# Optimization experiments

Measured on AMD Instinct MI355X. Metric: run time of the kernel, lower is better.

## Reference

```python
import jax, jax.numpy as jnp
import numpy as np

NUM_HEADS = 16
NUM_KV_HEADS = 4
HEAD_DIM = 256
ROPE_THETA = 10000.0


def _rope(x, position_ids):
    # x: [B, H, S, D], position_ids: [B, S]
    d = x.shape[-1]
    inv_freq = 1.0 / (ROPE_THETA ** (jnp.arange(0, d, 2, dtype=jnp.float32) / d))  # [D/2]
    freqs = position_ids.astype(jnp.float32)[:, :, None] * inv_freq[None, None, :]  # [B, S, D/2]
    emb = jnp.concatenate([freqs, freqs], axis=-1)  # [B, S, D]
    cos = jnp.cos(emb)[:, None, :, :]
    sin = jnp.sin(emb)[:, None, :, :]
    x1, x2 = jnp.split(x, 2, axis=-1)
    rot = jnp.concatenate([-x2, x1], axis=-1)
    return x * cos + rot * sin


def setup_inputs() -> dict:
    key = jax.random.key(0)
    k1, k2, k3, k4, k5 = jax.random.split(key, 5)
    B, S, H = 2, 2048, 2048
    hidden_states = jax.random.normal(k1, (B, S, H), dtype=jnp.float32)
    position_ids = jnp.broadcast_to(jnp.arange(S, dtype=jnp.int32)[None, :], (B, S))
    scale = 1.0 / np.sqrt(H)
    wq = jax.random.normal(k2, (H, NUM_HEADS * HEAD_DIM), dtype=jnp.float32) * scale
    wk = jax.random.normal(k3, (H, NUM_KV_HEADS * HEAD_DIM), dtype=jnp.float32) * scale
    wv = jax.random.normal(k4, (H, NUM_KV_HEADS * HEAD_DIM), dtype=jnp.float32) * scale
    wo = jax.random.normal(k5, (NUM_HEADS * HEAD_DIM, H), dtype=jnp.float32) * (1.0 / np.sqrt(NUM_HEADS * HEAD_DIM))
    return {"hidden_states": hidden_states, "position_ids": position_ids,
            "wq": wq, "wk": wk, "wv": wv, "wo": wo}


def reference(hidden_states, position_ids, wq, wk, wv, wo):
    B, S, H = hidden_states.shape
    groups = NUM_HEADS // NUM_KV_HEADS
    # QKV projections -> [B, heads, S, D]
    q = (hidden_states @ wq).reshape(B, S, NUM_HEADS, HEAD_DIM).transpose(0, 2, 1, 3)
    k = (hidden_states @ wk).reshape(B, S, NUM_KV_HEADS, HEAD_DIM).transpose(0, 2, 1, 3)
    v = (hidden_states @ wv).reshape(B, S, NUM_KV_HEADS, HEAD_DIM).transpose(0, 2, 1, 3)
    q = _rope(q, position_ids)
    k = _rope(k, position_ids)
    # GQA without materializing repeated K/V: group query heads per kv head
    qg = q.reshape(B, NUM_KV_HEADS, groups, S, HEAD_DIM)
    scale = 1.0 / jnp.sqrt(jnp.asarray(HEAD_DIM, dtype=q.dtype))
    scores = jnp.einsum('bkgqd,bkvd->bkgqv', qg, k) * scale  # [B, KV, G, S, S]
    causal = jnp.tril(jnp.ones((S, S), dtype=bool))
    scores = jnp.where(causal[None, None, None, :, :], scores, jnp.finfo(scores.dtype).min)
    probs = jax.nn.softmax(scores, axis=-1)
    out = jnp.einsum('bkgqv,bkvd->bkgqd', probs, v)  # [B, KV, G, S, D]
    out = out.reshape(B, NUM_HEADS, S, HEAD_DIM).transpose(0, 2, 1, 3).reshape(B, S, NUM_HEADS * HEAD_DIM)
    return out @ wo
```

## Files before the change

kernel.cpp:

```cpp
#include <hip/hip_runtime.h>

typedef unsigned short u16;
typedef __bf16 bf16_t;
typedef bf16_t bf16x8 __attribute__((ext_vector_type(8)));
typedef float f32x4 __attribute__((ext_vector_type(4)));
typedef float f32x16 __attribute__((ext_vector_type(16)));

#define LOG2E 1.4426950408889634f
#define QKVS 6144

__device__ __forceinline__ u16 f2bf(float f) {
  union { float f; unsigned u; } c; c.f = f;
  unsigned r = c.u + 0x7fffu + ((c.u >> 16) & 1u);
  return (u16)(r >> 16);
}
__device__ __forceinline__ float bf2f(u16 u) {
  union { unsigned u; float f; } c; c.u = ((unsigned)u) << 16;
  return c.f;
}

__device__ __forceinline__ void gload16(const void* g, void* l) {
  __builtin_amdgcn_global_load_lds(
      (const __attribute__((address_space(1))) unsigned int*)g,
      (__attribute__((address_space(3))) unsigned int*)l, 16, 0, 0);
}

__device__ __forceinline__ unsigned cvtpk(float lo, float hi) {
  unsigned r;
  asm("v_cvt_pk_bf16_f32 %0, %1, %2" : "=v"(r) : "v"(lo), "v"(hi));
  return r;
}
__device__ __forceinline__ void swap32(unsigned& a, unsigned& b) {
  asm("v_permlane32_swap_b32 %0, %1" : "+v"(a), "+v"(b));
}

#define MFMA16(a, b, c) __builtin_amdgcn_mfma_f32_16x16x32_bf16((a), (b), (c), 0, 0, 0)
#define MFMA32(a, b, c) __builtin_amdgcn_mfma_f32_32x32x16_bf16((a), (b), (c), 0, 0, 0)


__global__ __launch_bounds__(256) void k_convert_f32_bf16(const float* __restrict__ in,
                                                          u16* __restrict__ out, int n4) {
  int i = blockIdx.x * 256 + threadIdx.x;
  if (i >= n4) return;
  float4 v = ((const float4*)in)[i];
  ushort4 o;
  o.x = f2bf(v.x); o.y = f2bf(v.y); o.z = f2bf(v.z); o.w = f2bf(v.w);
  ((ushort4*)out)[i] = o;
}

__global__ __launch_bounds__(256) void k_transpose_all(const float* __restrict__ wq,
                                                       const float* __restrict__ wk,
                                                       const float* __restrict__ wv,
                                                       const float* __restrict__ wo,
                                                       u16* __restrict__ Wqkvt,
                                                       u16* __restrict__ Wot) {
  __shared__ float tile[32][33];
  int fb = blockIdx.x;
  const float* in;
  u16* out;
  int R, C, bxi, byi;
  if (fb < 8192) {
    in = wq; out = Wqkvt; R = 2048; C = 4096;
    bxi = fb & 127; byi = fb >> 7;
  } else if (fb < 10240) {
    in = wk; out = Wqkvt + 4096 * 2048; R = 2048; C = 1024;
    int l = fb - 8192; bxi = l & 31; byi = l >> 5;
  } else if (fb < 12288) {
    in = wv; out = Wqkvt + 5120 * 2048; R = 2048; C = 1024;
    int l = fb - 10240; bxi = l & 31; byi = l >> 5;
  } else {
    in = wo; out = Wot; R = 4096; C = 2048;
    int l = fb - 12288; bxi = l & 63; byi = l >> 6;
  }
  int tx = threadIdx.x & 31, ty = threadIdx.x >> 5;
  int bx = bxi * 32, by = byi * 32;
#pragma unroll
  for (int i = 0; i < 4; i++)
    tile[ty + i * 8][tx] = in[(size_t)(by + ty + i * 8) * C + bx + tx];
  __syncthreads();
#pragma unroll
  for (int i = 0; i < 4; i++)
    out[(size_t)(bx + ty + i * 8) * R + by + tx] = f2bf(tile[tx][ty + i * 8]);
}

__global__ __launch_bounds__(256) void k_transpose_bf16(const u16* __restrict__ in,
                                                        u16* __restrict__ out, int R, int C) {
  __shared__ u16 tile[32][33];
  int tx = threadIdx.x, ty = threadIdx.y;
  int bx = blockIdx.x * 32, by = blockIdx.y * 32;
#pragma unroll
  for (int i = 0; i < 4; i++)
    tile[ty + i * 8][tx] = in[(size_t)(by + ty + i * 8) * C + bx + tx];
  __syncthreads();
#pragma unroll
  for (int i = 0; i < 4; i++)
    out[(size_t)(bx + ty + i * 8) * R + by + tx] = tile[tx][ty + i * 8];
}

__global__ __launch_bounds__(256) void k_ropetab(const int* __restrict__ pos,
                                                 float2* __restrict__ tab) {
  int idx = blockIdx.x * 256 + threadIdx.x;
  int i = idx & 127, row = idx >> 7;
  float p = (float)pos[row];
  float f = p * exp2f((float)i * (-13.287712379549449f / 128.f));
  float sn, cs;
  sincosf(f, &sn, &cs);
  tab[idx] = make_float2(cs, sn);
}


template <int OUT_BF16>
__global__ __launch_bounds__(256) void k_gemm_bt(const u16* __restrict__ A,
                                                 const u16* __restrict__ Bt,
                                                 void* __restrict__ C, int M, int N, int K) {
  __shared__ u16 As[128 * 64];
  __shared__ u16 Bs[128 * 64];
  const int tid = threadIdx.x;
  const int lane = tid & 63;
  const int w = tid >> 6;
  const int l15 = lane & 15, l4 = lane >> 4;
  const int wr = w >> 1, wc = w & 1;
  const int bx = blockIdx.x, by = blockIdx.y;

  f32x4 acc[4][4];
#pragma unroll
  for (int a = 0; a < 4; a++)
#pragma unroll
    for (int b2 = 0; b2 < 4; b2++) acc[a][b2] = (f32x4){0.f, 0.f, 0.f, 0.f};

  const u16* Abase = A + (size_t)by * 128 * K;
  const u16* Bbase = Bt + (size_t)bx * 128 * K;

  for (int kk = 0; kk < K; kk += 64) {
    __syncthreads();
#pragma unroll
    for (int j = 0; j < 4; j++) {
      int ci = w * 256 + j * 64 + lane;
      int row = ci >> 3, c = ci & 7;
      gload16(Abase + (size_t)row * K + kk + c * 8, (char*)As + ci * 16);
      gload16(Bbase + (size_t)row * K + kk + c * 8, (char*)Bs + ci * 16);
    }
    __syncthreads();
#pragma unroll
    for (int kc = 0; kc < 2; kc++) {
      int kb = kc * 64 + l4 * 16;
      bf16x8 av[4], bv[4];
#pragma unroll
      for (int mt = 0; mt < 4; mt++)
        av[mt] = *(const bf16x8*)((const char*)As + (wr * 64 + mt * 16 + l15) * 128 + kb);
#pragma unroll
      for (int nt = 0; nt < 4; nt++)
        bv[nt] = *(const bf16x8*)((const char*)Bs + (wc * 64 + nt * 16 + l15) * 128 + kb);
#pragma unroll
      for (int mt = 0; mt < 4; mt++)
#pragma unroll
        for (int nt = 0; nt < 4; nt++) acc[mt][nt] = MFMA16(av[mt], bv[nt], acc[mt][nt]);
    }
  }
#pragma unroll
  for (int mt = 0; mt < 4; mt++) {
#pragma unroll
    for (int nt = 0; nt < 4; nt++) {
      int col = bx * 128 + wc * 64 + nt * 16 + l15;
#pragma unroll
      for (int r = 0; r < 4; r++) {
        int row = by * 128 + wr * 64 + mt * 16 + l4 * 4 + r;
        if (OUT_BF16)
          ((u16*)C)[(size_t)row * N + col] = f2bf(acc[mt][nt][r]);
        else
          ((float*)C)[(size_t)row * N + col] = acc[mt][nt][r];
      }
    }
  }
}


__global__ __launch_bounds__(512, 1) void k_gemm256(const u16* __restrict__ A,
                                                    const u16* __restrict__ Bt,
                                                    u16* __restrict__ C, int N, int K,
                                                    const float2* __restrict__ tab) {
  extern __shared__ char smem[];
  const int tid = threadIdx.x;
  const int lane = tid & 63, w = tid >> 6;
  const int l15 = lane & 15, l4 = lane >> 4;
  const int wr = w >> 2, wc = w & 3;
  const int bx = blockIdx.x, by = blockIdx.y;
  const int NT = K >> 6;

  const u16* Ab = A + (size_t)(by * 256) * K;
  const u16* Bb = Bt + (size_t)(bx * 256) * K;

  int srcoff[2], dstoff[2];
#pragma unroll
  for (int rr = 0; rr < 2; rr++) {
    int ci = rr * 512 + tid;
    int lc = ci ^ (((ci >> 5) & 1) << 1);
    int kc = lc >> 9, row = (lc >> 2) & 127, g2 = lc & 3;
    srcoff[rr] = row * K + kc * 32 + g2 * 8;
    dstoff[rr] = ci * 16;
  }

  auto SH = [&](int Tg, int halfidx) {
    const u16* base = (halfidx < 2) ? (Ab + (size_t)(halfidx * 128) * K)
                                    : (Bb + (size_t)((halfidx - 2) * 128) * K);
    char* dst = smem + (Tg & 1) * 65536 + halfidx * 16384;
    int kk = Tg * 64;
#pragma unroll
    for (int rr = 0; rr < 2; rr++)
      gload16(base + srcoff[rr] + kk, dst + dstoff[rr]);
  };

  auto lda = [&](int c, int kc, int mrow4) -> bf16x8 {
    int L = kc * 8192 + (mrow4 * 16 + l15) * 64 + l4 * 16;
    int P = L ^ (((L >> 9) & 1) << 5);
    return *(const bf16x8*)(smem + c * 65536 + wr * 16384 + P);
  };
  auto ldb = [&](int c, int kc, int j) -> bf16x8 {
    int L = kc * 8192 + ((wc & 1) * 64 + j * 16 + l15) * 64 + l4 * 16;
    int P = L ^ (((L >> 9) & 1) << 5);
    return *(const bf16x8*)(smem + c * 65536 + 32768 + (wc >> 1) * 16384 + P);
  };

  f32x4 acc[8][4];
#pragma unroll
  for (int i = 0; i < 8; i++)
#pragma unroll
    for (int j = 0; j < 4; j++) acc[i][j] = (f32x4){0.f, 0.f, 0.f, 0.f};

  SH(0, 0); SH(0, 1); SH(0, 2); SH(0, 3);
  SH(1, 2); SH(1, 3);
  asm volatile("s_waitcnt vmcnt(4)" ::: "memory");
  __builtin_amdgcn_s_barrier();
  asm volatile("" ::: "memory");

  bf16x8 bv[2][4];
  for (int T = 0; T < NT; ++T) {
    const int c = T & 1;
#pragma unroll
    for (int q = 0; q < 4; q++) {
      const int kc = q & 1, mh = q >> 1;
      bf16x8 av[4];
      if (q < 2) {
#pragma unroll
        for (int j = 0; j < 4; j++) bv[kc][j] = ldb(c, kc, j);
      }
#pragma unroll
      for (int ii = 0; ii < 4; ii++) av[ii] = lda(c, kc, mh * 4 + ii);
      if (q == 0)      { if (T + 1 < NT) SH(T + 1, 0); }
      else if (q == 1) { if (T + 1 < NT) SH(T + 1, 1); }
      else if (q == 2) { if (T + 2 < NT) SH(T + 2, 2); }
      else             { if (T + 2 < NT) SH(T + 2, 3); }
      if (q == 3) {
        if (T < NT - 2)       asm volatile("s_waitcnt vmcnt(4)" ::: "memory");
        else if (T == NT - 2) asm volatile("s_waitcnt vmcnt(0)" ::: "memory");
      }
      asm volatile("" ::: "memory");
      __builtin_amdgcn_s_barrier();
      asm volatile("" ::: "memory");
      asm volatile("s_waitcnt lgkmcnt(0)" ::: "memory");
      __builtin_amdgcn_sched_barrier(0);
      __builtin_amdgcn_s_setprio(1);
#pragma unroll
      for (int ii = 0; ii < 4; ii++)
#pragma unroll
        for (int j = 0; j < 4; j++)
          acc[mh * 4 + ii][j] = MFMA16(av[ii], bv[kc][j], acc[mh * 4 + ii][j]);
      __builtin_amdgcn_s_setprio(0);
      asm volatile("" ::: "memory");
      __builtin_amdgcn_s_barrier();
      asm volatile("" ::: "memory");
    }
  }

  if (bx < 20) {
    float4* X4 = (float4*)smem;
    const float sgn = (wc < 2) ? -1.f : 1.f;
    const int ptid = tid ^ 128;
#pragma unroll
    for (int ih = 0; ih < 2; ih++) {
      __syncthreads();
#pragma unroll
      for (int i2 = 0; i2 < 4; i2++)
#pragma unroll
        for (int j2 = 0; j2 < 4; j2++) {
          f32x4 a = acc[ih * 4 + i2][j2];
          X4[(i2 * 4 + j2) * 512 + tid] = make_float4(a[0], a[1], a[2], a[3]);
        }
      __syncthreads();
#pragma unroll
      for (int i2 = 0; i2 < 4; i2++) {
#pragma unroll
        for (int j2 = 0; j2 < 4; j2++) {
          int col = bx * 256 + wc * 64 + j2 * 16 + l15;
          int ti = (wc & 1) * 64 + j2 * 16 + l15;
          float4 part = X4[(i2 * 4 + j2) * 512 + ptid];
          float pa[4] = {part.x, part.y, part.z, part.w};
#pragma unroll
          for (int r2 = 0; r2 < 4; r2++) {
            int row = by * 256 + wr * 128 + (ih * 4 + i2) * 16 + l4 * 4 + r2;
            float mine = acc[ih * 4 + i2][j2][r2];
            float2 t = tab[(size_t)row * 128 + ti];
            C[(size_t)row * N + col] = f2bf(mine * t.x + sgn * pa[r2] * t.y);
          }
        }
      }
    }
  } else {
#pragma unroll
    for (int i = 0; i < 8; i++) {
#pragma unroll
      for (int j = 0; j < 4; j++) {
        int col = bx * 256 + wc * 64 + j * 16 + l15;
#pragma unroll
        for (int r = 0; r < 4; r++) {
          int row = by * 256 + wr * 128 + i * 16 + l4 * 4 + r;
          C[(size_t)row * N + col] = f2bf(acc[i][j][r]);
        }
      }
    }
  }
}


__shared__ __align__(16) u16 aK0[8192];
__shared__ __align__(16) u16 aK1[8192];
__shared__ __align__(16) u16 aV0[8192];
__shared__ __align__(16) u16 aV1[8192];

__global__ __launch_bounds__(256, 2) void k_attn(const u16* __restrict__ QKV,
                                                 const u16* __restrict__ Vt,
                                                 u16* __restrict__ AO) {
  const int tid = threadIdx.x, lane = tid & 63, w = tid >> 6;
  const int r31 = lane & 31, hi = lane >> 5;

  const int flat = blockIdx.x;
  const int r = flat & 7;
  const int idx = flat >> 3;
  const int b = r >> 2, kv = r & 3;
  const int half = idx >> 5, j = idx & 31;
  const int qb = half ? 15 - (j >> 1) : (j >> 1);
  const int h = kv * 4 + (j & 1) + 2 * half;

  bf16x8 qreg[16];
  {
    const u16* qp = QKV + (size_t)(b * 2048 + qb * 128 + w * 32 + r31) * QKVS + h * 256 + hi * 8;
#pragma unroll
    for (int kc = 0; kc < 16; kc++) qreg[kc] = *(const bf16x8*)(qp + kc * 16);
  }

  f32x16 o[8];
#pragma unroll
  for (int df = 0; df < 8; df++)
#pragma unroll
    for (int jj = 0; jj < 16; jj++) o[df][jj] = 0.f;
  float mrow = -3e38f, lrow = 0.f;

  const int nt = 4 * qb + 4;
  const int tlim = 4 * qb + w;
  const int qloc = qb * 128 + w * 32 + r31;
  const u16* Kbase = QKV + (size_t)(b * 2048) * QKVS + 4096 + kv * 256;
  const u16* Vbase = Vt + (size_t)(kv * 256) * 4096 + b * 2048;

  int kfix[4], vfix[4];
#pragma unroll
  for (int jj = 0; jj < 4; jj++) {
    int ci = jj * 256 + tid;
    int krow = ci >> 5, kc = ci & 31;
    int kcg = (kc & 24) | ((kc ^ krow) & 7);
    kfix[jj] = krow * QKVS + kcg * 8;
    int vrow = ci >> 2, vc = ci & 3;
    int vg = (vc - (vrow >> 1)) & 3;
    vfix[jj] = vrow * 4096 + vg * 8;
  }
  int koff = 0, voff = 0;

  auto STAGE = [&](u16* Kd, u16* Vd) {
#pragma unroll
    for (int jj = 0; jj < 4; jj++)
      gload16(Kbase + kfix[jj] + koff, (char*)Kd + (jj * 256 + tid) * 16);
#pragma unroll
    for (int jj = 0; jj < 4; jj++)
      gload16(Vbase + vfix[jj] + voff, (char*)Vd + (jj * 256 + tid) * 16);
    koff += 32 * QKVS;
    voff += 32;
  };

  auto COMPUTE = [&](int t, const u16* Kc, const u16* Vc) {
    f32x16 s;
#pragma unroll
    for (int jj = 0; jj < 16; jj++) s[jj] = 0.f;
#pragma unroll
    for (int kc = 0; kc < 16; kc++) {
      int ch = kc * 2 + hi;
      int cs = (ch & 24) | ((ch ^ r31) & 7);
      bf16x8 kf = *(const bf16x8*)((const char*)Kc + r31 * 512 + cs * 16);
      s = MFMA32(kf, qreg[kc], s);
    }

    const float C = 0.0625f * LOG2E;
    float z[16];
#pragma unroll
    for (int jj = 0; jj < 16; jj++) z[jj] = s[jj] * C;
    if (t == tlim) {
#pragma unroll
      for (int jj = 0; jj < 16; jj++) {
        int kvg = t * 32 + (jj & 3) + 8 * (jj >> 2) + 4 * hi;
        if (kvg > qloc) z[jj] = -1e30f;
      }
    }

    float m0 = z[0];
#pragma unroll
    for (int jj = 1; jj < 16; jj++) m0 = fmaxf(m0, z[jj]);
    m0 = fmaxf(m0, __shfl_xor(m0, 32));
    if (__any(m0 > mrow + 11.54f)) {
      float mn = fmaxf(mrow, m0);
      float alpha = exp2f(mrow - mn);
      mrow = mn;
      lrow *= alpha;
#pragma unroll
      for (int jj = 0; jj < 16; jj++) {
        float a = __shfl(alpha, (jj & 3) + 8 * (jj >> 2) + 4 * hi);
#pragma unroll
        for (int df = 0; df < 8; df++) o[df][jj] *= a;
      }
    }
    float sum = 0.f;
#pragma unroll
    for (int jj = 0; jj < 16; jj++) {
      z[jj] = exp2f(z[jj] - mrow);
      sum += z[jj];
    }
    sum += __shfl_xor(sum, 32);
    lrow += sum;

    unsigned a0 = cvtpk(z[0], z[1]), a2 = cvtpk(z[4], z[5]);
    swap32(a0, a2);
    unsigned a1 = cvtpk(z[2], z[3]), a3 = cvtpk(z[6], z[7]);
    swap32(a1, a3);
    unsigned b0 = cvtpk(z[8], z[9]), b2 = cvtpk(z[12], z[13]);
    swap32(b0, b2);
    unsigned b1 = cvtpk(z[10], z[11]), b3 = cvtpk(z[14], z[15]);
    swap32(b1, b3);
    union UU { unsigned u[4]; bf16x8 v; };
    UU ua; ua.u[0] = a0; ua.u[1] = a1; ua.u[2] = a2; ua.u[3] = a3;
    UU ub; ub.u[0] = b0; ub.u[1] = b1; ub.u[2] = b2; ub.u[3] = b3;
    bf16x8 pa0 = ua.v, pa1 = ub.v;

#pragma unroll
    for (int df = 0; df < 8; df++) {
      int vr = df * 32 + r31;
      int c0 = (hi + (vr >> 1)) & 3;
      int c1 = (2 + hi + (vr >> 1)) & 3;
      bf16x8 v0 = *(const bf16x8*)((const char*)Vc + vr * 64 + c0 * 16);
      bf16x8 v1 = *(const bf16x8*)((const char*)Vc + vr * 64 + c1 * 16);
      o[df] = MFMA32(pa0, v0, o[df]);
      o[df] = MFMA32(pa1, v1, o[df]);
    }
  };

  STAGE(aK0, aV0);
  __syncthreads();

  for (int t = 0; t < nt; t += 2) {
    STAGE(aK1, aV1);
    if (t <= tlim) COMPUTE(t, aK0, aV0);
    __syncthreads();
    if (t + 2 < nt) STAGE(aK0, aV0);
    if (t + 1 <= tlim) COMPUTE(t + 1, aK1, aV1);
    __syncthreads();
  }

  float rl = 1.f / lrow;
  size_t rowbase = (size_t)(b * 2048 + qb * 128 + w * 32);
#pragma unroll
  for (int jj = 0; jj < 16; jj++) {
    float rr2 = __shfl(rl, (jj & 3) + 8 * (jj >> 2) + 4 * hi);
    int qr = (jj & 3) + 8 * (jj >> 2) + 4 * hi;
#pragma unroll
    for (int df = 0; df < 8; df++)
      AO[(rowbase + qr) * 4096 + h * 256 + df * 32 + r31] = f2bf(o[df][jj] * rr2);
  }
}


#define OFF_AO    0u
#define OFF_XB    0u
#define OFF_WQKVT 16777216u
#define OFF_VT    33554432u
#define OFF_WOT   41943040u
#define OFF_QKV   58720256u
#define OFF_TAB   109051904u

extern "C" void kernel_launch(void* const* d_in, const int* in_sizes, int n_in,
                              void* d_out, int out_size, void* d_ws, size_t ws_size,
                              hipStream_t stream) {
  const float* hs = (const float*)d_in[0];
  const int* pos = (const int*)d_in[1];
  const float* wq = (const float*)d_in[2];
  const float* wk = (const float*)d_in[3];
  const float* wv = (const float*)d_in[4];
  const float* wo = (const float*)d_in[5];
  float* out = (float*)d_out;
  char* ws = (char*)d_ws;

  u16* Xb    = (u16*)(ws + OFF_XB);
  u16* Wqkvt = (u16*)(ws + OFF_WQKVT);
  u16* Vt    = (u16*)(ws + OFF_VT);
  u16* Wot   = (u16*)(ws + OFF_WOT);
  u16* QKV   = (u16*)(ws + OFF_QKV);
  float2* Tab = (float2*)(ws + OFF_TAB);
  u16* AO    = (u16*)(ws + OFF_AO);

  dim3 tb(32, 8);

  k_ropetab<<<2048, 256, 0, stream>>>(pos, Tab);

  k_convert_f32_bf16<<<8192, 256, 0, stream>>>(hs, Xb, 2097152);
  k_transpose_all<<<20480, 256, 0, stream>>>(wq, wk, wv, wo, Wqkvt, Wot);

  (void)hipFuncSetAttribute((const void*)k_gemm256,
                            hipFuncAttributeMaxDynamicSharedMemorySize, 131072);
  k_gemm256<<<dim3(24, 16), 512, 131072, stream>>>(Xb, Wqkvt, QKV, 6144, 2048, Tab);

  k_transpose_bf16<<<dim3(32, 128), tb, 0, stream>>>(QKV + 5120, Vt, 4096, QKVS);

  k_attn<<<dim3(512), 256, 0, stream>>>(QKV, Vt, AO);

  k_gemm_bt<0><<<dim3(16, 32), 256, 0, stream>>>(AO, Wot, out, 4096, 2048, 4096);
}
```

Baseline: 466.9 us.

## Fuse prep kernels into one launch and write V transposed from QKV GEMM epilogue

Merges the hidden-state conversion, weight transposes and RoPE table kernels into a single k_prep launch. The QKV GEMM epilogue for V column blocks now stages accumulators through LDS and writes V directly in transposed layout to a new Vt buffer, so the separate bf16 transpose kernel is gone. This removes two launches and a full read and write of V, at the cost of extra LDS traffic and syncs in the epilogue. The V tiles are no longer written to QKV, which is fine only if attention reads V solely from Vt.

```diff
diff --git a/kernel.cpp b/kernel.cpp
--- a/kernel.cpp
+++ b/kernel.cpp
@@ -37,40 +37,51 @@
 #define MFMA16(a, b, c) __builtin_amdgcn_mfma_f32_16x16x32_bf16((a), (b), (c), 0, 0, 0)
 #define MFMA32(a, b, c) __builtin_amdgcn_mfma_f32_32x32x16_bf16((a), (b), (c), 0, 0, 0)
 
-
-__global__ __launch_bounds__(256) void k_convert_f32_bf16(const float* __restrict__ in,
-                                                          u16* __restrict__ out, int n4) {
-  int i = blockIdx.x * 256 + threadIdx.x;
-  if (i >= n4) return;
-  float4 v = ((const float4*)in)[i];
-  ushort4 o;
-  o.x = f2bf(v.x); o.y = f2bf(v.y); o.z = f2bf(v.z); o.w = f2bf(v.w);
-  ((ushort4*)out)[i] = o;
-}
-
-__global__ __launch_bounds__(256) void k_transpose_all(const float* __restrict__ wq,
-                                                       const float* __restrict__ wk,
-                                                       const float* __restrict__ wv,
-                                                       const float* __restrict__ wo,
-                                                       u16* __restrict__ Wqkvt,
-                                                       u16* __restrict__ Wot) {
+__global__ __launch_bounds__(256) void k_prep(const float* __restrict__ hs,
+                                              const int* __restrict__ pos,
+                                              const float* __restrict__ wq,
+                                              const float* __restrict__ wk,
+                                              const float* __restrict__ wv,
+                                              const float* __restrict__ wo,
+                                              u16* __restrict__ Xb,
+                                              u16* __restrict__ Wqkvt,
+                                              u16* __restrict__ Wot,
+                                              float2* __restrict__ tab) {
   __shared__ float tile[32][33];
-  int fb = blockIdx.x;
+  const int fb = blockIdx.x;
+  if (fb < 8192) {
+    int i = fb * 256 + threadIdx.x;
+    float4 v = ((const float4*)hs)[i];
+    ushort4 o;
+    o.x = f2bf(v.x); o.y = f2bf(v.y); o.z = f2bf(v.z); o.w = f2bf(v.w);
+    ((ushort4*)Xb)[i] = o;
+    return;
+  }
+  if (fb >= 28672) {
+    int idx = (fb - 28672) * 256 + threadIdx.x;
+    int i = idx & 127, row = idx >> 7;
+    float p = (float)pos[row];
+    float f = p * exp2f((float)i * (-13.287712379549449f / 128.f));
+    float sn, cs;
+    sincosf(f, &sn, &cs);
+    tab[idx] = make_float2(cs, sn);
+    return;
+  }
   const float* in;
   u16* out;
   int R, C, bxi, byi;
-  if (fb < 8192) {
+  if (fb < 16384) {
     in = wq; out = Wqkvt; R = 2048; C = 4096;
-    bxi = fb & 127; byi = fb >> 7;
-  } else if (fb < 10240) {
+    int l = fb - 8192; bxi = l & 127; byi = l >> 7;
+  } else if (fb < 18432) {
     in = wk; out = Wqkvt + 4096 * 2048; R = 2048; C = 1024;
-    int l = fb - 8192; bxi = l & 31; byi = l >> 5;
-  } else if (fb < 12288) {
+    int l = fb - 16384; bxi = l & 31; byi = l >> 5;
+  } else if (fb < 20480) {
     in = wv; out = Wqkvt + 5120 * 2048; R = 2048; C = 1024;
-    int l = fb - 10240; bxi = l & 31; byi = l >> 5;
+    int l = fb - 18432; bxi = l & 31; byi = l >> 5;
   } else {
     in = wo; out = Wot; R = 4096; C = 2048;
-    int l = fb - 12288; bxi = l & 63; byi = l >> 6;
+    int l = fb - 20480; bxi = l & 63; byi = l >> 6;
   }
   int tx = threadIdx.x & 31, ty = threadIdx.x >> 5;
   int bx = bxi * 32, by = byi * 32;
@@ -81,31 +92,6 @@
 #pragma unroll
   for (int i = 0; i < 4; i++)
     out[(size_t)(bx + ty + i * 8) * R + by + tx] = f2bf(tile[tx][ty + i * 8]);
-}
-
-__global__ __launch_bounds__(256) void k_transpose_bf16(const u16* __restrict__ in,
-                                                        u16* __restrict__ out, int R, int C) {
-  __shared__ u16 tile[32][33];
-  int tx = threadIdx.x, ty = threadIdx.y;
-  int bx = blockIdx.x * 32, by = blockIdx.y * 32;
-#pragma unroll
-  for (int i = 0; i < 4; i++)
-    tile[ty + i * 8][tx] = in[(size_t)(by + ty + i * 8) * C + bx + tx];
-  __syncthreads();
-#pragma unroll
-  for (int i = 0; i < 4; i++)
-    out[(size_t)(bx + ty + i * 8) * R + by + tx] = tile[tx][ty + i * 8];
-}
-
-__global__ __launch_bounds__(256) void k_ropetab(const int* __restrict__ pos,
-                                                 float2* __restrict__ tab) {
-  int idx = blockIdx.x * 256 + threadIdx.x;
-  int i = idx & 127, row = idx >> 7;
-  float p = (float)pos[row];
-  float f = p * exp2f((float)i * (-13.287712379549449f / 128.f));
-  float sn, cs;
-  sincosf(f, &sn, &cs);
-  tab[idx] = make_float2(cs, sn);
 }
 
 
@@ -178,7 +164,8 @@
 __global__ __launch_bounds__(512, 1) void k_gemm256(const u16* __restrict__ A,
                                                     const u16* __restrict__ Bt,
                                                     u16* __restrict__ C, int N, int K,
-                                                    const float2* __restrict__ tab) {
+                                                    const float2* __restrict__ tab,
+                                                    u16* __restrict__ Vt) {
   extern __shared__ char smem[];
   const int tid = threadIdx.x;
   const int lane = tid & 63, w = tid >> 6;
@@ -306,16 +293,31 @@
       }
     }
   } else {
-#pragma unroll
-    for (int i = 0; i < 8; i++) {
-#pragma unroll
-      for (int j = 0; j < 4; j++) {
-        int col = bx * 256 + wc * 64 + j * 16 + l15;
-#pragma unroll
-        for (int r = 0; r < 4; r++) {
-          int row = by * 256 + wr * 128 + i * 16 + l4 * 4 + r;
-          C[(size_t)row * N + col] = f2bf(acc[i][j][r]);
+    u16* lt = (u16*)smem;
+    const int vbase = bx * 256 - 5120;
+#pragma unroll
+    for (int ih = 0; ih < 2; ih++) {
+      __syncthreads();
+#pragma unroll
+      for (int i2 = 0; i2 < 4; i2++) {
+#pragma unroll
+        for (int j2 = 0; j2 < 4; j2++) {
+          int col = wc * 64 + j2 * 16 + l15;
+          int lrow = wr * 64 + i2 * 16 + l4 * 4;
+          f32x4 a = acc[ih * 4 + i2][j2];
+          ushort4 pk;
+          pk.x = f2bf(a[0]); pk.y = f2bf(a[1]); pk.z = f2bf(a[2]); pk.w = f2bf(a[3]);
+          *(ushort4*)&lt[col * 136 + lrow] = pk;
         }
+      }
+      __syncthreads();
+#pragma unroll
+      for (int v = 0; v < 8; v++) {
+        int idx2 = v * 512 + tid;
+        int vc = idx2 >> 4, tv = idx2 & 15;
+        bf16x8 val = *(const bf16x8*)&lt[vc * 136 + tv * 8];
+        int token = by * 256 + ((tv < 8) ? (ih * 64 + tv * 8) : (128 + ih * 64 + (tv - 8) * 8));
+        *(bf16x8*)&Vt[(size_t)(vbase + vc) * 4096 + token] = val;
       }
     }
   }
@@ -487,10 +489,10 @@
 #define OFF_AO    0u
 #define OFF_XB    0u
 #define OFF_WQKVT 16777216u
-#define OFF_VT    33554432u
 #define OFF_WOT   41943040u
 #define OFF_QKV   58720256u
 #define OFF_TAB   109051904u
+#define OFF_VT    113246208u
 
 extern "C" void kernel_launch(void* const* d_in, const int* in_sizes, int n_in,
                               void* d_out, int out_size, void* d_ws, size_t ws_size,
@@ -506,24 +508,17 @@
 
   u16* Xb    = (u16*)(ws + OFF_XB);
   u16* Wqkvt = (u16*)(ws + OFF_WQKVT);
-  u16* Vt    = (u16*)(ws + OFF_VT);
   u16* Wot   = (u16*)(ws + OFF_WOT);
   u16* QKV   = (u16*)(ws + OFF_QKV);
   float2* Tab = (float2*)(ws + OFF_TAB);
+  u16* Vt    = (u16*)(ws + OFF_VT);
   u16* AO    = (u16*)(ws + OFF_AO);
 
-  dim3 tb(32, 8);
-
-  k_ropetab<<<2048, 256, 0, stream>>>(pos, Tab);
-
-  k_convert_f32_bf16<<<8192, 256, 0, stream>>>(hs, Xb, 2097152);
-  k_transpose_all<<<20480, 256, 0, stream>>>(wq, wk, wv, wo, Wqkvt, Wot);
+  k_prep<<<30720, 256, 0, stream>>>(hs, pos, wq, wk, wv, wo, Xb, Wqkvt, Wot, Tab);
 
   (void)hipFuncSetAttribute((const void*)k_gemm256,
                             hipFuncAttributeMaxDynamicSharedMemorySize, 131072);
-  k_gemm256<<<dim3(24, 16), 512, 131072, stream>>>(Xb, Wqkvt, QKV, 6144, 2048, Tab);
-
-  k_transpose_bf16<<<dim3(32, 128), tb, 0, stream>>>(QKV + 5120, Vt, 4096, QKVS);
+  k_gemm256<<<dim3(24, 16), 512, 131072, stream>>>(Xb, Wqkvt, QKV, 6144, 2048, Tab, Vt);
 
   k_attn<<<dim3(512), 256, 0, stream>>>(QKV, Vt, AO);
 
```

Measured after the change: 453.8 us. 1.03x faster.
